# Kernel optimization log

Measured on AMD Instinct MI355X. Metric: run time of the kernel, lower is better.

The kernel has to match this reference:

```python
import jax, jax.numpy as jnp
import numpy as np

HEADS = 16
S = 1024      # affine_dim
B, L = 4, 2048


def _conv1x1(x, W, b):
    # Conv1d with kernel_size=1: pointwise channel mixing. x: (B, C, L)
    return jnp.einsum('oc,bcl->bol', W, x) + b[None, :, None]


def setup_inputs() -> dict:
    key = jax.random.key(0)
    ks = jax.random.split(key, 7)
    scale = 1.0 / np.sqrt(S)  # ~ torch Conv1d default init scale
    return {
        'x':  jax.random.normal(ks[0], (B, S, L), dtype=jnp.float32),
        'Wk': jax.random.normal(ks[1], (S, S), dtype=jnp.float32) * scale,
        'bk': jax.random.normal(ks[2], (S,), dtype=jnp.float32) * scale,
        'Wq': jax.random.normal(ks[3], (S, S), dtype=jnp.float32) * scale,
        'bq': jax.random.normal(ks[4], (S,), dtype=jnp.float32) * scale,
        'Wp': jax.random.normal(ks[5], (S, S), dtype=jnp.float32) * scale,
        'bp': jax.random.normal(ks[6], (S,), dtype=jnp.float32) * scale,
    }


def reference(x, Wk, bk, Wq, bq, Wp, bp):
    b, c, l = x.shape
    h = HEADS
    d = c // h
    keys = _conv1x1(x, Wk, bk).reshape(b, h, d, l)
    queries = _conv1x1(x, Wq, bq).reshape(b, h, d, l)
    # scores[b,h,i,j] = sum_d keys[...,d,i] * queries[...,d,j]  (keys^T @ queries)
    # NOTE: original scales by `seqlen ** 1 / 2` == seqlen / 2 (Python precedence),
    # i.e. multiply by 2/L, NOT 1/sqrt(L). Faithfully preserved.
    scores = jnp.einsum('bhdi,bhdj->bhij', keys, queries) * (2.0 / l)
    attn = jax.nn.softmax(scores, axis=-1)
    xh = x.reshape(b, h, d, l)  # raw x used as values
    out = jnp.einsum('bhdi,bhij->bhdj', xh, attn).reshape(b, c, l)
    return _conv1x1(out, Wp, bp)
```

## Files before the change

kernel.cpp:

```cpp
#include <hip/hip_runtime.h>
#include <hip/hip_bf16.h>
#include <cstdint>
#include <cstddef>

#ifndef __has_builtin
#define __has_builtin(x) 0
#endif

#define DEVI __device__ __forceinline__

typedef __attribute__((ext_vector_type(8))) __bf16 bf16x8;
typedef __attribute__((ext_vector_type(4))) float float4v;
typedef __attribute__((ext_vector_type(16))) float float16v;
typedef __attribute__((ext_vector_type(4))) unsigned short ushort4v;
typedef __attribute__((ext_vector_type(4))) unsigned int uint4v;

constexpr int Bd = 4, Sd = 1024, Ld = 2048, Hd = 16, Dd = 64;

DEVI unsigned short f2bf(float x){
  union { float f; unsigned u; } v; v.f = x;
  unsigned r = v.u + 0x7fffu + ((v.u >> 16) & 1u);
  return (unsigned short)(r >> 16);
}

DEVI unsigned pack2(float lo, float hi){
  union { float f; unsigned u; } a, b; a.f = lo; b.f = hi;
  unsigned ra = a.u + 0x8000u;
  unsigned rb = b.u + 0x8000u;
#if __has_builtin(__builtin_amdgcn_perm)
  return __builtin_amdgcn_perm(rb, ra, 0x07060302u);
#else
  return (ra >> 16) | (rb & 0xffff0000u);
#endif
}

DEVI float fast_exp2(float x){
#if __has_builtin(__builtin_amdgcn_exp2f)
  return __builtin_amdgcn_exp2f(x);
#else
  return exp2f(x);
#endif
}

DEVI void plane32_swap(unsigned &a, unsigned &b){
  asm("v_permlane32_swap_b32 %0, %1" : "+v"(a), "+v"(b));
}

DEVI void gload_lds16(const void* g, void* lds){
  __builtin_amdgcn_global_load_lds(
      (const __attribute__((address_space(1))) void*)g,
      (__attribute__((address_space(3))) void*)lds,
      16, 0, 0);
}

DEVI float4v mfma_bf16(bf16x8 a, bf16x8 b, float4v c){
  return __builtin_amdgcn_mfma_f32_16x16x32_bf16(a, b, c, 0, 0, 0);
}

DEVI float16v mfma32_bf16(bf16x8 a, bf16x8 b, float16v c){
  return __builtin_amdgcn_mfma_f32_32x32x16_bf16(a, b, c, 0, 0, 0);
}


__global__ void wcast_kernel(const float* __restrict__ Wk, const float* __restrict__ Wq,
                             const float* __restrict__ Wp,
                             unsigned short* __restrict__ Wkbf, unsigned short* __restrict__ Wqbf,
                             unsigned short* __restrict__ Wpbf, float ck){
  size_t i = ((size_t)blockIdx.x * 256 + threadIdx.x) * 4;
  float4v a = *(const float4v*)(Wk + i);
  float4v b = *(const float4v*)(Wq + i);
  float4v c = *(const float4v*)(Wp + i);
  ushort4v oa = { f2bf(a[0]*ck), f2bf(a[1]*ck), f2bf(a[2]*ck), f2bf(a[3]*ck) };
  ushort4v ob = { f2bf(b[0]), f2bf(b[1]), f2bf(b[2]), f2bf(b[3]) };
  ushort4v oc = { f2bf(c[0]), f2bf(c[1]), f2bf(c[2]), f2bf(c[3]) };
  *(ushort4v*)(Wkbf + i) = oa;
  *(ushort4v*)(Wqbf + i) = ob;
  *(ushort4v*)(Wpbf + i) = oc;
}

__global__ void transpose_cast(const float* __restrict__ x, unsigned short* __restrict__ Xt){
  __shared__ float tile[32][33];
  const int b = blockIdx.z;
  const int l0 = blockIdx.x * 32;
  const int s0 = blockIdx.y * 32;
  const int tx = threadIdx.x, ty = threadIdx.y;
  #pragma unroll
  for (int r = 0; r < 32; r += 8)
    tile[ty + r][tx] = x[((size_t)b*Sd + s0 + ty + r)*Ld + l0 + tx];
  __syncthreads();
  #pragma unroll
  for (int r = 0; r < 32; r += 8)
    Xt[((size_t)b*Ld + l0 + ty + r)*Sd + s0 + tx] = f2bf(tile[tx][ty + r]);
}

__global__ void vprime_kernel(const float* __restrict__ x, const float* __restrict__ invZ,
                              unsigned short* __restrict__ Vp){
  size_t idx = ((size_t)blockIdx.x * 256 + threadIdx.x) * 4;
  const int l = (int)(idx & (Ld - 1));
  const int c = (int)((idx >> 11) & (Sd - 1));
  const int b = (int)(idx >> 21);
  const int h = c >> 6;
  float4v xv = *(const float4v*)(x + idx);
  float4v zv = *(const float4v*)(invZ + ((size_t)(b*Hd + h) * Ld + l));
  ushort4v o = { f2bf(xv[0]*zv[0]), f2bf(xv[1]*zv[1]), f2bf(xv[2]*zv[2]), f2bf(xv[3]*zv[3]) };
  *(ushort4v*)(Vp + idx) = o;
}

template<int OUT_MODE>
__global__ __launch_bounds__(256, 2)
void conv_gemm(const unsigned short* __restrict__ A,
               const unsigned short* __restrict__ Bt,
               const float* __restrict__ bias, float bscale,
               unsigned short* __restrict__ outT,
               float* __restrict__ outF)
{
  constexpr int BK = 32;
  constexpr int NKSTEP = Sd / BK;
  __shared__ __attribute__((aligned(16))) unsigned short Abuf[2][128*BK];
  __shared__ __attribute__((aligned(16))) unsigned short Bbuf[2][128*BK];

  const int b  = blockIdx.z;
  const int n0 = blockIdx.x * 128;
  const int m0 = blockIdx.y * 128;
  const int tid = threadIdx.x;
  const int w = tid >> 6, lane = tid & 63, lr = lane & 15, lg = lane >> 4;
  const int wm = (w >> 1) * 64, wn = (w & 1) * 64;

  const unsigned short* Abase = A + (size_t)m0 * Sd;
  const unsigned short* Bbase = Bt + ((size_t)b * Ld + n0) * Sd;

  auto stage = [&](int bf, int kt){
    #pragma unroll
    for (int p = 0; p < 2; ++p){
      int slot = p*256 + tid;
      int row = slot >> 2, c = slot & 3;
      int csrc = c ^ ((row >> 1) & 3);
      gload_lds16(Abase + (size_t)row * Sd + kt*BK + csrc*8,
                  (void*)(&Abuf[bf][(size_t)(p*256 + w*64) * 8]));
    }
    #pragma unroll
    for (int p = 0; p < 2; ++p){
      int slot = p*256 + tid;
      int row = slot >> 2, c = slot & 3;
      int csrc = c ^ ((row >> 1) & 3);
      gload_lds16(Bbase + (size_t)row * Sd + kt*BK + csrc*8,
                  (void*)(&Bbuf[bf][(size_t)(p*256 + w*64) * 8]));
    }
  };

  const int gsw = lg ^ ((lr >> 1) & 3);

  float4v acc[4][4];
  #pragma unroll
  for (int i = 0; i < 4; ++i)
    #pragma unroll
    for (int j = 0; j < 4; ++j)
      acc[i][j] = (float4v){0.f, 0.f, 0.f, 0.f};

  stage(0, 0);
  __syncthreads();
  int cur = 0;
  for (int kt = 0; kt < NKSTEP; ++kt){
    if (kt + 1 < NKSTEP) stage(cur ^ 1, kt + 1);
    bf16x8 af[4], bfv[4];
    #pragma unroll
    for (int i = 0; i < 4; ++i){
      int row = wm + i*16 + lr;
      af[i] = *(const bf16x8*)((const char*)&Abuf[cur][0] + (size_t)row*64 + gsw*16);
    }
    #pragma unroll
    for (int j = 0; j < 4; ++j){
      int row = wn + j*16 + lr;
      bfv[j] = *(const bf16x8*)((const char*)&Bbuf[cur][0] + (size_t)row*64 + gsw*16);
    }
    #pragma unroll
    for (int i = 0; i < 4; ++i)
      #pragma unroll
      for (int j = 0; j < 4; ++j)
        acc[i][j] = mfma_bf16(af[i], bfv[j], acc[i][j]);
    __syncthreads();
    cur ^= 1;
  }

  #pragma unroll
  for (int i = 0; i < 4; ++i){
    const int mb = m0 + wm + i*16 + lg*4;
    float4v bv = *(const float4v*)(bias + mb);
    #pragma unroll
    for (int j = 0; j < 4; ++j){
      const int n = n0 + wn + j*16 + lr;
      float4v v = acc[i][j];
      float o0 = v[0] + bscale*bv[0];
      float o1 = v[1] + bscale*bv[1];
      float o2 = v[2] + bscale*bv[2];
      float o3 = v[3] + bscale*bv[3];
      if (OUT_MODE == 0){
        ushort4v o = { f2bf(o0), f2bf(o1), f2bf(o2), f2bf(o3) };
        *(ushort4v*)(outT + ((size_t)b*Ld + n)*Sd + mb) = o;
      } else {
        outF[((size_t)b*Sd + mb + 0)*Ld + n] = o0;
        outF[((size_t)b*Sd + mb + 1)*Ld + n] = o1;
        outF[((size_t)b*Sd + mb + 2)*Ld + n] = o2;
        outF[((size_t)b*Sd + mb + 3)*Ld + n] = o3;
      }
    }
  }
}

__global__ __launch_bounds__(256, 2)
void conv_gemm_kq(const unsigned short* __restrict__ Ak,
                  const unsigned short* __restrict__ Aq,
                  const unsigned short* __restrict__ Bt,
                  const float* __restrict__ bk, const float* __restrict__ bq,
                  float ck,
                  unsigned short* __restrict__ Kt,
                  unsigned short* __restrict__ Qt)
{
  constexpr int BK = 32;
  constexpr int NKSTEP = Sd / BK;
  __shared__ __attribute__((aligned(16))) unsigned short AbufK[2][128*BK];
  __shared__ __attribute__((aligned(16))) unsigned short AbufQ[2][128*BK];
  __shared__ __attribute__((aligned(16))) unsigned short Bbuf[2][128*BK];

  const int b  = blockIdx.z;
  const int n0 = blockIdx.x * 128;
  const int m0 = blockIdx.y * 128;
  const int tid = threadIdx.x;
  const int w = tid >> 6, lane = tid & 63, lr = lane & 15, lg = lane >> 4;
  const int wm = (w >> 1) * 64, wn = (w & 1) * 64;

  const unsigned short* AKbase = Ak + (size_t)m0 * Sd;
  const unsigned short* AQbase = Aq + (size_t)m0 * Sd;
  const unsigned short* Bbase  = Bt + ((size_t)b * Ld + n0) * Sd;

  auto stage = [&](int bf, int kt){
    #pragma unroll
    for (int p = 0; p < 2; ++p){
      int slot = p*256 + tid;
      int row = slot >> 2, c = slot & 3;
      int csrc = c ^ ((row >> 1) & 3);
      const size_t soff = (size_t)row * Sd + kt*BK + csrc*8;
      void* dk = (void*)(&AbufK[bf][(size_t)(p*256 + w*64) * 8]);
      void* dq = (void*)(&AbufQ[bf][(size_t)(p*256 + w*64) * 8]);
      void* db = (void*)(&Bbuf [bf][(size_t)(p*256 + w*64) * 8]);
      gload_lds16(AKbase + soff, dk);
      gload_lds16(AQbase + soff, dq);
      gload_lds16(Bbase  + soff, db);
    }
  };

  const int gsw = lg ^ ((lr >> 1) & 3);

  float4v acck[4][4], accq[4][4];
  #pragma unroll
  for (int i = 0; i < 4; ++i)
    #pragma unroll
    for (int j = 0; j < 4; ++j){
      acck[i][j] = (float4v){0.f, 0.f, 0.f, 0.f};
      accq[i][j] = (float4v){0.f, 0.f, 0.f, 0.f};
    }

  stage(0, 0);
  __syncthreads();
  int cur = 0;
  for (int kt = 0; kt < NKSTEP; ++kt){
    if (kt + 1 < NKSTEP) stage(cur ^ 1, kt + 1);
    bf16x8 afk[4], afq[4], bfv[4];
    #pragma unroll
    for (int i = 0; i < 4; ++i){
      int row = wm + i*16 + lr;
      afk[i] = *(const bf16x8*)((const char*)&AbufK[cur][0] + (size_t)row*64 + gsw*16);
      afq[i] = *(const bf16x8*)((const char*)&AbufQ[cur][0] + (size_t)row*64 + gsw*16);
    }
    #pragma unroll
    for (int j = 0; j < 4; ++j){
      int row = wn + j*16 + lr;
      bfv[j] = *(const bf16x8*)((const char*)&Bbuf[cur][0] + (size_t)row*64 + gsw*16);
    }
    #pragma unroll
    for (int i = 0; i < 4; ++i)
      #pragma unroll
      for (int j = 0; j < 4; ++j){
        acck[i][j] = mfma_bf16(afk[i], bfv[j], acck[i][j]);
        accq[i][j] = mfma_bf16(afq[i], bfv[j], accq[i][j]);
      }
    __syncthreads();
    cur ^= 1;
  }

  #pragma unroll
  for (int i = 0; i < 4; ++i){
    const int mb = m0 + wm + i*16 + lg*4;
    float4v bkv = *(const float4v*)(bk + mb);
    float4v bqv = *(const float4v*)(bq + mb);
    #pragma unroll
    for (int j = 0; j < 4; ++j){
      const int n = n0 + wn + j*16 + lr;
      float4v vk = acck[i][j];
      float4v vq = accq[i][j];
      ushort4v ok = { f2bf(vk[0] + ck*bkv[0]), f2bf(vk[1] + ck*bkv[1]),
                      f2bf(vk[2] + ck*bkv[2]), f2bf(vk[3] + ck*bkv[3]) };
      ushort4v oq = { f2bf(vq[0] + bqv[0]), f2bf(vq[1] + bqv[1]),
                      f2bf(vq[2] + bqv[2]), f2bf(vq[3] + bqv[3]) };
      *(ushort4v*)(Kt + ((size_t)b*Ld + n)*Sd + mb) = ok;
      *(ushort4v*)(Qt + ((size_t)b*Ld + n)*Sd + mb) = oq;
    }
  }
}

__global__ __launch_bounds__(256, 4)
void stats_kernel(const unsigned short* __restrict__ Kt,
                  const unsigned short* __restrict__ Qt,
                  float* __restrict__ invZ)
{
  __shared__ __attribute__((aligned(16))) unsigned short Qbuf[2][64*64];

  const int m = blockIdx.x;
  const int xcd = m & 7, slot = m >> 3;
  const int bh = xcd * 8 + (slot >> 3);
  const int ib = slot & 7;
  const int b = bh >> 4, h = bh & 15;
  const int i0 = ib * 256;

  const int tid = threadIdx.x, w = tid >> 6, lane = tid & 63;
  const int l31 = lane & 31, lh = lane >> 5;
  const int iw0 = i0 + w * 64;

  bf16x8 kb[2][4];
  #pragma unroll
  for (int is = 0; is < 2; ++is)
    #pragma unroll
    for (int ks = 0; ks < 4; ++ks)
      kb[is][ks] = *(const bf16x8*)(Kt + ((size_t)b*Ld + iw0 + is*32 + l31)*Sd + h*64 + ks*16 + lh*8);

  const size_t qbase = (size_t)b*Ld*Sd + (size_t)h*64;
  auto stage = [&](int bf, int jt){
    const int j0 = jt * 64;
    #pragma unroll
    for (int p = 0; p < 2; ++p){
      const int slot2 = p*256 + tid;
      const int row = slot2 >> 3;
      const int gsrc = (slot2 & 7) ^ (row & 7);
      gload_lds16(Qt + qbase + (size_t)(j0 + row)*Sd + gsrc*8,
                  (void*)(&Qbuf[bf][(size_t)slot2 * 8]));
    }
  };

  float z[2] = {0.f, 0.f};
  stage(0, 0);
  __syncthreads();
  int cur = 0;
  for (int jt = 0; jt < 32; ++jt){
    if (jt + 1 < 32) stage(cur ^ 1, jt + 1);
    #pragma unroll
    for (int js = 0; js < 2; ++js){
      bf16x8 qf[4];
      #pragma unroll
      for (int ks = 0; ks < 4; ++ks){
        const int row = js*32 + l31;
        const int g = (2*ks + lh) ^ (l31 & 7);
        qf[ks] = *(const bf16x8*)((const char*)&Qbuf[cur][0] + (size_t)row*128 + g*16);
      }
      #pragma unroll
      for (int is = 0; is < 2; ++is){
        float16v sacc;
        #pragma unroll
        for (int r = 0; r < 16; ++r) sacc[r] = 0.f;
        __builtin_amdgcn_s_setprio(1);
        #pragma unroll
        for (int ks = 0; ks < 4; ++ks)
          sacc = mfma32_bf16(qf[ks], kb[is][ks], sacc);
        __builtin_amdgcn_s_setprio(0);
        #pragma unroll
        for (int r = 0; r < 16; ++r) z[is] += fast_exp2(sacc[r]);
      }
    }
    __syncthreads();
    cur ^= 1;
  }

  #pragma unroll
  for (int is = 0; is < 2; ++is){
    float zv = z[is] + __shfl_xor(z[is], 32, 64);
    if (lh == 0)
      invZ[(size_t)bh * Ld + iw0 + is*32 + l31] = 1.0f / zv;
  }
}

__global__ __launch_bounds__(256, 2)
void attn_pv_kernel(const unsigned short* __restrict__ Kt,
                    const unsigned short* __restrict__ Qt,
                    const unsigned short* __restrict__ Vp,
                    unsigned short* __restrict__ AOt)
{
  __shared__ __attribute__((aligned(16))) unsigned short Kbuf[2][64*64];
  __shared__ __attribute__((aligned(16))) unsigned short Vbuf[2][64*64];

  const int m = blockIdx.x;
  const int xcd = m & 7, slot = m >> 3;
  const int bh = xcd * 8 + (slot >> 3);
  const int jb = slot & 7;
  const int b = bh >> 4, h = bh & 15;
  const int j0 = jb * 256;

  const int tid = threadIdx.x, w = tid >> 6, lane = tid & 63;
  const int l31 = lane & 31, lh = lane >> 5;
  const int jw = j0 + w * 64;

  bf16x8 qb[2][4];
  #pragma unroll
  for (int js = 0; js < 2; ++js)
    #pragma unroll
    for (int ks = 0; ks < 4; ++ks)
      qb[js][ks] = *(const bf16x8*)(Qt + ((size_t)b*Ld + jw + js*32 + l31)*Sd + h*64 + ks*16 + lh*8);

  float16v oacc[2][2];
  #pragma unroll
  for (int ds = 0; ds < 2; ++ds)
    #pragma unroll
    for (int js = 0; js < 2; ++js)
      #pragma unroll
      for (int r = 0; r < 16; ++r) oacc[ds][js][r] = 0.f;

  const size_t kbase = (size_t)b*Ld*Sd + (size_t)h*64;
  const size_t vbase = ((size_t)b*Sd + h*64)*Ld;

  auto stage = [&](int bf, int it){
    const int i0 = it * 64;
    #pragma unroll
    for (int p = 0; p < 2; ++p){
      const int slot2 = p*256 + tid;
      const int row = slot2 >> 3;
      const int gsrc = (slot2 & 7) ^ (row & 7);
      gload_lds16(Kt + kbase + (size_t)(i0 + row)*Sd + gsrc*8,
                  (void*)(&Kbuf[bf][(size_t)slot2 * 8]));
      gload_lds16(Vp + vbase + (size_t)row*Ld + i0 + gsrc*8,
                  (void*)(&Vbuf[bf][(size_t)slot2 * 8]));
    }
  };

  bf16x8 kf[2][4], vf[2][4];
  float16v sacc[2];
  float16v sacc2[2][2];

  auto read_kf = [&](int cb){
    #pragma unroll
    for (int is = 0; is < 2; ++is)
      #pragma unroll
      for (int ks = 0; ks < 4; ++ks){
        const int row = is*32 + l31;
        const int g = (2*ks + lh) ^ (l31 & 7);
        kf[is][ks] = *(const bf16x8*)((const char*)&Kbuf[cb][0] + (size_t)row*128 + g*16);
      }
  };
  auto read_vf = [&](int cb){
    #pragma unroll
    for (int is = 0; is < 2; ++is)
      #pragma unroll
      for (int ks = 0; ks < 4; ++ks){
        const int row = is*32 + l31;
        const int g = (2*ks + lh) ^ (l31 & 7);
        vf[is][ks] = *(const bf16x8*)((const char*)&Vbuf[cb][0] + (size_t)row*128 + g*16);
      }
  };
  auto do_qk = [&](){
    #pragma unroll
    for (int is = 0; is < 2; ++is)
      #pragma unroll
      for (int js = 0; js < 2; ++js)
        #pragma unroll
        for (int r = 0; r < 16; ++r) sacc2[is][js][r] = 0.f;
    __builtin_amdgcn_s_setprio(1);
    #pragma unroll
    for (int js = 0; js < 2; ++js)
      #pragma unroll
      for (int is = 0; is < 2; ++is)
        #pragma unroll
        for (int ks = 0; ks < 4; ++ks)
          sacc2[is][js] = mfma32_bf16(kf[is][ks], qb[js][ks], sacc2[is][js]);
    __builtin_amdgcn_s_setprio(0);
  };
  auto do_exp_pv = [&](){
    #pragma unroll
    for (int js = 0; js < 2; ++js){
      bf16x8 pf[4];
      #pragma unroll
      for (int is = 0; is < 2; ++is){
        #pragma unroll
        for (int hs = 0; hs < 2; ++hs){
          const int r0 = 8*hs;
          unsigned W0 = pack2(fast_exp2(sacc2[is][js][r0+0]), fast_exp2(sacc2[is][js][r0+1]));
          unsigned W1 = pack2(fast_exp2(sacc2[is][js][r0+2]), fast_exp2(sacc2[is][js][r0+3]));
          unsigned W2 = pack2(fast_exp2(sacc2[is][js][r0+4]), fast_exp2(sacc2[is][js][r0+5]));
          unsigned W3 = pack2(fast_exp2(sacc2[is][js][r0+6]), fast_exp2(sacc2[is][js][r0+7]));
          plane32_swap(W0, W2);
          plane32_swap(W1, W3);
          union { uint4v u; bf16x8 v; } cvt;
          cvt.u = (uint4v){ W0, W1, W2, W3 };
          pf[is*2 + hs] = cvt.v;
        }
      }
      __builtin_amdgcn_s_setprio(1);
      #pragma unroll
      for (int kp = 0; kp < 4; ++kp)
        #pragma unroll
        for (int ds = 0; ds < 2; ++ds)
          oacc[ds][js] = mfma32_bf16(vf[ds][kp], pf[kp], oacc[ds][js]);
      __builtin_amdgcn_s_setprio(0);
    }
  };

  stage(0, 0);
  __syncthreads();
  stage(1, 1);
  read_kf(0);
  do_qk();
  read_vf(0);

  for (int t = 0; t < 31; ++t){
    __syncthreads();
    if (t < 30) stage((t) & 1, t + 2);
    read_kf((t + 1) & 1);
    do_exp_pv();
    do_qk();
    read_vf((t + 1) & 1);
  }
  do_exp_pv();

  #pragma unroll
  for (int ds = 0; ds < 2; ++ds)
    #pragma unroll
    for (int js = 0; js < 2; ++js)
      #pragma unroll
      for (int rq = 0; rq < 4; ++rq){
        const int d0 = ds*32 + 8*rq + 4*lh;
        ushort4v o = { f2bf(oacc[ds][js][4*rq+0]), f2bf(oacc[ds][js][4*rq+1]),
                       f2bf(oacc[ds][js][4*rq+2]), f2bf(oacc[ds][js][4*rq+3]) };
        *(ushort4v*)(AOt + ((size_t)b*Ld + jw + js*32 + l31)*Sd + h*64 + d0) = o;
      }
}


extern "C" void kernel_launch(void* const* d_in, const int* in_sizes, int n_in,
                              void* d_out, int out_size, void* d_ws, size_t ws_size,
                              hipStream_t stream)
{
  const float* x  = (const float*)d_in[0];
  const float* Wk = (const float*)d_in[1];
  const float* bk = (const float*)d_in[2];
  const float* Wq = (const float*)d_in[3];
  const float* bq = (const float*)d_in[4];
  const float* Wp = (const float*)d_in[5];
  const float* bp = (const float*)d_in[6];
  float* out = (float*)d_out;

  char* ws = (char*)d_ws;
  const size_t SZ_BLS = (size_t)Bd * Ld * Sd * 2;
  unsigned short* Xt   = (unsigned short*)(ws);
  unsigned short* Kt   = (unsigned short*)(ws + SZ_BLS);
  unsigned short* Qt   = (unsigned short*)(ws + 2*SZ_BLS);
  unsigned short* AOt  = (unsigned short*)(ws + 3*SZ_BLS);
  unsigned short* Wkbf = (unsigned short*)(ws + 4*SZ_BLS);
  unsigned short* Wqbf = (unsigned short*)(ws + 4*SZ_BLS + (size_t)2097152);
  unsigned short* Wpbf = (unsigned short*)(ws + 4*SZ_BLS + (size_t)2*2097152);
  float* invZ          = (float*)(ws + 4*SZ_BLS + (size_t)3*2097152);
  unsigned short* Vp   = Xt;

  const float ck = (2.0f / (float)Ld) * 1.44269504088896f;

  wcast_kernel<<<1024, 256, 0, stream>>>(Wk, Wq, Wp, Wkbf, Wqbf, Wpbf, ck);
  transpose_cast<<<dim3(Ld/32, Sd/32, Bd), dim3(32, 8), 0, stream>>>(x, Xt);

  dim3 cg(Ld/128, Sd/128, Bd);
  conv_gemm_kq<<<cg, 256, 0, stream>>>(Wkbf, Wqbf, Xt, bk, bq, ck, Kt, Qt);

  stats_kernel<<<dim3((Ld/256)*(Bd*Hd)), 256, 0, stream>>>(Kt, Qt, invZ);
  vprime_kernel<<<(Bd*(size_t)Sd*Ld/4)/256, 256, 0, stream>>>(x, invZ, Vp);
  attn_pv_kernel<<<dim3((Ld/256)*(Bd*Hd)), 256, 0, stream>>>(Kt, Qt, Vp, AOt);

  conv_gemm<1><<<cg, 256, 0, stream>>>(Wpbf, AOt, bp, 1.0f, nullptr, out);
}
```

Measured before the change: 218.2 us.

## Split attention over key range into two halves, reduce in projection GEMM

The attention-PV kernel now splits the summation over source positions i into two halves, doubling the grid. Each half writes a separate partial output buffer. The final projection GEMM runs its K loop over both buffers, which sums the partials for free since the projection is linear. This raises parallelism in the attention stage, which had only 512 blocks. The cost is an extra output buffer of workspace traffic, a doubled K loop in the projection GEMM, and bf16 rounding of each partial.

```diff
diff --git a/kernel.cpp b/kernel.cpp
--- a/kernel.cpp
+++ b/kernel.cpp
@@ -106,107 +106,6 @@
   *(ushort4v*)(Vp + idx) = o;
 }
 
-template<int OUT_MODE>
-__global__ __launch_bounds__(256, 2)
-void conv_gemm(const unsigned short* __restrict__ A,
-               const unsigned short* __restrict__ Bt,
-               const float* __restrict__ bias, float bscale,
-               unsigned short* __restrict__ outT,
-               float* __restrict__ outF)
-{
-  constexpr int BK = 32;
-  constexpr int NKSTEP = Sd / BK;
-  __shared__ __attribute__((aligned(16))) unsigned short Abuf[2][128*BK];
-  __shared__ __attribute__((aligned(16))) unsigned short Bbuf[2][128*BK];
-
-  const int b  = blockIdx.z;
-  const int n0 = blockIdx.x * 128;
-  const int m0 = blockIdx.y * 128;
-  const int tid = threadIdx.x;
-  const int w = tid >> 6, lane = tid & 63, lr = lane & 15, lg = lane >> 4;
-  const int wm = (w >> 1) * 64, wn = (w & 1) * 64;
-
-  const unsigned short* Abase = A + (size_t)m0 * Sd;
-  const unsigned short* Bbase = Bt + ((size_t)b * Ld + n0) * Sd;
-
-  auto stage = [&](int bf, int kt){
-    #pragma unroll
-    for (int p = 0; p < 2; ++p){
-      int slot = p*256 + tid;
-      int row = slot >> 2, c = slot & 3;
-      int csrc = c ^ ((row >> 1) & 3);
-      gload_lds16(Abase + (size_t)row * Sd + kt*BK + csrc*8,
-                  (void*)(&Abuf[bf][(size_t)(p*256 + w*64) * 8]));
-    }
-    #pragma unroll
-    for (int p = 0; p < 2; ++p){
-      int slot = p*256 + tid;
-      int row = slot >> 2, c = slot & 3;
-      int csrc = c ^ ((row >> 1) & 3);
-      gload_lds16(Bbase + (size_t)row * Sd + kt*BK + csrc*8,
-                  (void*)(&Bbuf[bf][(size_t)(p*256 + w*64) * 8]));
-    }
-  };
-
-  const int gsw = lg ^ ((lr >> 1) & 3);
-
-  float4v acc[4][4];
-  #pragma unroll
-  for (int i = 0; i < 4; ++i)
-    #pragma unroll
-    for (int j = 0; j < 4; ++j)
-      acc[i][j] = (float4v){0.f, 0.f, 0.f, 0.f};
-
-  stage(0, 0);
-  __syncthreads();
-  int cur = 0;
-  for (int kt = 0; kt < NKSTEP; ++kt){
-    if (kt + 1 < NKSTEP) stage(cur ^ 1, kt + 1);
-    bf16x8 af[4], bfv[4];
-    #pragma unroll
-    for (int i = 0; i < 4; ++i){
-      int row = wm + i*16 + lr;
-      af[i] = *(const bf16x8*)((const char*)&Abuf[cur][0] + (size_t)row*64 + gsw*16);
-    }
-    #pragma unroll
-    for (int j = 0; j < 4; ++j){
-      int row = wn + j*16 + lr;
-      bfv[j] = *(const bf16x8*)((const char*)&Bbuf[cur][0] + (size_t)row*64 + gsw*16);
-    }
-    #pragma unroll
-    for (int i = 0; i < 4; ++i)
-      #pragma unroll
-      for (int j = 0; j < 4; ++j)
-        acc[i][j] = mfma_bf16(af[i], bfv[j], acc[i][j]);
-    __syncthreads();
-    cur ^= 1;
-  }
-
-  #pragma unroll
-  for (int i = 0; i < 4; ++i){
-    const int mb = m0 + wm + i*16 + lg*4;
-    float4v bv = *(const float4v*)(bias + mb);
-    #pragma unroll
-    for (int j = 0; j < 4; ++j){
-      const int n = n0 + wn + j*16 + lr;
-      float4v v = acc[i][j];
-      float o0 = v[0] + bscale*bv[0];
-      float o1 = v[1] + bscale*bv[1];
-      float o2 = v[2] + bscale*bv[2];
-      float o3 = v[3] + bscale*bv[3];
-      if (OUT_MODE == 0){
-        ushort4v o = { f2bf(o0), f2bf(o1), f2bf(o2), f2bf(o3) };
-        *(ushort4v*)(outT + ((size_t)b*Ld + n)*Sd + mb) = o;
-      } else {
-        outF[((size_t)b*Sd + mb + 0)*Ld + n] = o0;
-        outF[((size_t)b*Sd + mb + 1)*Ld + n] = o1;
-        outF[((size_t)b*Sd + mb + 2)*Ld + n] = o2;
-        outF[((size_t)b*Sd + mb + 3)*Ld + n] = o3;
-      }
-    }
-  }
-}
-
 __global__ __launch_bounds__(256, 2)
 void conv_gemm_kq(const unsigned short* __restrict__ Ak,
                   const unsigned short* __restrict__ Aq,
@@ -308,6 +207,93 @@
   }
 }
 
+__global__ __launch_bounds__(256, 2)
+void conv_gemm_p(const unsigned short* __restrict__ A,
+                 const unsigned short* __restrict__ Bt0,
+                 const unsigned short* __restrict__ Bt1,
+                 const float* __restrict__ bias,
+                 float* __restrict__ outF)
+{
+  constexpr int BK = 32;
+  constexpr int NKSTEP = 64;
+  __shared__ __attribute__((aligned(16))) unsigned short Abuf[2][128*BK];
+  __shared__ __attribute__((aligned(16))) unsigned short Bbuf[2][128*BK];
+
+  const int b  = blockIdx.z;
+  const int n0 = blockIdx.x * 128;
+  const int m0 = blockIdx.y * 128;
+  const int tid = threadIdx.x;
+  const int w = tid >> 6, lane = tid & 63, lr = lane & 15, lg = lane >> 4;
+  const int wm = (w >> 1) * 64, wn = (w & 1) * 64;
+
+  const unsigned short* Abase  = A + (size_t)m0 * Sd;
+  const unsigned short* B0base = Bt0 + ((size_t)b * Ld + n0) * Sd;
+  const unsigned short* B1base = Bt1 + ((size_t)b * Ld + n0) * Sd;
+
+  auto stage = [&](int bf, int kt){
+    const int kk = kt & 31;
+    const unsigned short* Bb = (kt < 32) ? B0base : B1base;
+    #pragma unroll
+    for (int p = 0; p < 2; ++p){
+      int slot = p*256 + tid;
+      int row = slot >> 2, c = slot & 3;
+      int csrc = c ^ ((row >> 1) & 3);
+      const size_t soff = (size_t)row * Sd + kk*BK + csrc*8;
+      gload_lds16(Abase + soff, (void*)(&Abuf[bf][(size_t)(p*256 + w*64) * 8]));
+      gload_lds16(Bb    + soff, (void*)(&Bbuf[bf][(size_t)(p*256 + w*64) * 8]));
+    }
+  };
+
+  const int gsw = lg ^ ((lr >> 1) & 3);
+
+  float4v acc[4][4];
+  #pragma unroll
+  for (int i = 0; i < 4; ++i)
+    #pragma unroll
+    for (int j = 0; j < 4; ++j)
+      acc[i][j] = (float4v){0.f, 0.f, 0.f, 0.f};
+
+  stage(0, 0);
+  __syncthreads();
+  int cur = 0;
+  for (int kt = 0; kt < NKSTEP; ++kt){
+    if (kt + 1 < NKSTEP) stage(cur ^ 1, kt + 1);
+    bf16x8 af[4], bfv[4];
+    #pragma unroll
+    for (int i = 0; i < 4; ++i){
+      int row = wm + i*16 + lr;
+      af[i] = *(const bf16x8*)((const char*)&Abuf[cur][0] + (size_t)row*64 + gsw*16);
+    }
+    #pragma unroll
+    for (int j = 0; j < 4; ++j){
+      int row = wn + j*16 + lr;
+      bfv[j] = *(const bf16x8*)((const char*)&Bbuf[cur][0] + (size_t)row*64 + gsw*16);
+    }
+    #pragma unroll
+    for (int i = 0; i < 4; ++i)
+      #pragma unroll
+      for (int j = 0; j < 4; ++j)
+        acc[i][j] = mfma_bf16(af[i], bfv[j], acc[i][j]);
+    __syncthreads();
+    cur ^= 1;
+  }
+
+  #pragma unroll
+  for (int i = 0; i < 4; ++i){
+    const int mb = m0 + wm + i*16 + lg*4;
+    float4v bv = *(const float4v*)(bias + mb);
+    #pragma unroll
+    for (int j = 0; j < 4; ++j){
+      const int n = n0 + wn + j*16 + lr;
+      float4v v = acc[i][j];
+      outF[((size_t)b*Sd + mb + 0)*Ld + n] = v[0] + bv[0];
+      outF[((size_t)b*Sd + mb + 1)*Ld + n] = v[1] + bv[1];
+      outF[((size_t)b*Sd + mb + 2)*Ld + n] = v[2] + bv[2];
+      outF[((size_t)b*Sd + mb + 3)*Ld + n] = v[3] + bv[3];
+    }
+  }
+}
+
 __global__ __launch_bounds__(256, 4)
 void stats_kernel(const unsigned short* __restrict__ Kt,
                   const unsigned short* __restrict__ Qt,
@@ -391,21 +377,26 @@
 void attn_pv_kernel(const unsigned short* __restrict__ Kt,
                     const unsigned short* __restrict__ Qt,
                     const unsigned short* __restrict__ Vp,
-                    unsigned short* __restrict__ AOt)
+                    unsigned short* __restrict__ AOt0,
+                    unsigned short* __restrict__ AOt1)
 {
   __shared__ __attribute__((aligned(16))) unsigned short Kbuf[2][64*64];
   __shared__ __attribute__((aligned(16))) unsigned short Vbuf[2][64*64];
 
   const int m = blockIdx.x;
   const int xcd = m & 7, slot = m >> 3;
-  const int bh = xcd * 8 + (slot >> 3);
+  const int bh = xcd * 8 + (slot >> 4);
+  const int ih = (slot >> 3) & 1;
   const int jb = slot & 7;
   const int b = bh >> 4, h = bh & 15;
   const int j0 = jb * 256;
+  const int it0 = ih * 16;
 
   const int tid = threadIdx.x, w = tid >> 6, lane = tid & 63;
   const int l31 = lane & 31, lh = lane >> 5;
   const int jw = j0 + w * 64;
+
+  unsigned short* AOt = ih ? AOt1 : AOt0;
 
   bf16x8 qb[2][4];
   #pragma unroll
@@ -440,7 +431,6 @@
   };
 
   bf16x8 kf[2][4], vf[2][4];
-  float16v sacc[2];
   float16v sacc2[2][2];
 
   auto read_kf = [&](int cb){
@@ -510,16 +500,16 @@
     }
   };
 
-  stage(0, 0);
+  stage(0, it0 + 0);
   __syncthreads();
-  stage(1, 1);
+  stage(1, it0 + 1);
   read_kf(0);
   do_qk();
   read_vf(0);
 
-  for (int t = 0; t < 31; ++t){
+  for (int t = 0; t < 15; ++t){
     __syncthreads();
-    if (t < 30) stage((t) & 1, t + 2);
+    if (t < 14) stage(t & 1, it0 + t + 2);
     read_kf((t + 1) & 1);
     do_exp_pv();
     do_qk();
@@ -559,11 +549,12 @@
   unsigned short* Xt   = (unsigned short*)(ws);
   unsigned short* Kt   = (unsigned short*)(ws + SZ_BLS);
   unsigned short* Qt   = (unsigned short*)(ws + 2*SZ_BLS);
-  unsigned short* AOt  = (unsigned short*)(ws + 3*SZ_BLS);
-  unsigned short* Wkbf = (unsigned short*)(ws + 4*SZ_BLS);
-  unsigned short* Wqbf = (unsigned short*)(ws + 4*SZ_BLS + (size_t)2097152);
-  unsigned short* Wpbf = (unsigned short*)(ws + 4*SZ_BLS + (size_t)2*2097152);
-  float* invZ          = (float*)(ws + 4*SZ_BLS + (size_t)3*2097152);
+  unsigned short* AOt0 = (unsigned short*)(ws + 3*SZ_BLS);
+  unsigned short* AOt1 = (unsigned short*)(ws + 4*SZ_BLS);
+  unsigned short* Wkbf = (unsigned short*)(ws + 5*SZ_BLS);
+  unsigned short* Wqbf = (unsigned short*)(ws + 5*SZ_BLS + (size_t)2097152);
+  unsigned short* Wpbf = (unsigned short*)(ws + 5*SZ_BLS + (size_t)2*2097152);
+  float* invZ          = (float*)(ws + 5*SZ_BLS + (size_t)3*2097152);
   unsigned short* Vp   = Xt;
 
   const float ck = (2.0f / (float)Ld) * 1.44269504088896f;
@@ -576,7 +567,7 @@
 
   stats_kernel<<<dim3((Ld/256)*(Bd*Hd)), 256, 0, stream>>>(Kt, Qt, invZ);
   vprime_kernel<<<(Bd*(size_t)Sd*Ld/4)/256, 256, 0, stream>>>(x, invZ, Vp);
-  attn_pv_kernel<<<dim3((Ld/256)*(Bd*Hd)), 256, 0, stream>>>(Kt, Qt, Vp, AOt);
-
-  conv_gemm<1><<<cg, 256, 0, stream>>>(Wpbf, AOt, bp, 1.0f, nullptr, out);
-}
+  attn_pv_kernel<<<dim3(2*(Ld/256)*(Bd*Hd)), 256, 0, stream>>>(Kt, Qt, Vp, AOt0, AOt1);
+
+  conv_gemm_p<<<cg, 256, 0, stream>>>(Wpbf, AOt0, AOt1, bp, out);
+}
```

Result: slower. 238.7 us (+9.4%).

## Fuse V-prime scaling into stats kernel and vectorize transpose-cast

Applied to the files above, without the earlier changes.

Removes the separate vprime kernel by having each stats block write its 1/Z values to shared memory and then scale and cast its slice of x into Vp. This eliminates the invZ global buffer round trip and one kernel launch. The transpose kernel also switches to float4 loads and 4-wide bf16 stores with a 1D block. The fused epilogue adds x reads to the stats kernel, which may lengthen its tail.

```diff
diff --git a/kernel.cpp b/kernel.cpp
--- a/kernel.cpp
+++ b/kernel.cpp
@@ -83,27 +83,20 @@
   const int b = blockIdx.z;
   const int l0 = blockIdx.x * 32;
   const int s0 = blockIdx.y * 32;
-  const int tx = threadIdx.x, ty = threadIdx.y;
-  #pragma unroll
-  for (int r = 0; r < 32; r += 8)
-    tile[ty + r][tx] = x[((size_t)b*Sd + s0 + ty + r)*Ld + l0 + tx];
+  const int t = threadIdx.x;
+  {
+    const int r = t >> 3, c4 = (t & 7) * 4;
+    float4v v = *(const float4v*)(x + ((size_t)b*Sd + s0 + r)*Ld + l0 + c4);
+    tile[r][c4+0] = v[0]; tile[r][c4+1] = v[1];
+    tile[r][c4+2] = v[2]; tile[r][c4+3] = v[3];
+  }
   __syncthreads();
-  #pragma unroll
-  for (int r = 0; r < 32; r += 8)
-    Xt[((size_t)b*Ld + l0 + ty + r)*Sd + s0 + tx] = f2bf(tile[tx][ty + r]);
-}
-
-__global__ void vprime_kernel(const float* __restrict__ x, const float* __restrict__ invZ,
-                              unsigned short* __restrict__ Vp){
-  size_t idx = ((size_t)blockIdx.x * 256 + threadIdx.x) * 4;
-  const int l = (int)(idx & (Ld - 1));
-  const int c = (int)((idx >> 11) & (Sd - 1));
-  const int b = (int)(idx >> 21);
-  const int h = c >> 6;
-  float4v xv = *(const float4v*)(x + idx);
-  float4v zv = *(const float4v*)(invZ + ((size_t)(b*Hd + h) * Ld + l));
-  ushort4v o = { f2bf(xv[0]*zv[0]), f2bf(xv[1]*zv[1]), f2bf(xv[2]*zv[2]), f2bf(xv[3]*zv[3]) };
-  *(ushort4v*)(Vp + idx) = o;
+  {
+    const int l = t >> 3, g4 = (t & 7) * 4;
+    ushort4v o = { f2bf(tile[g4+0][l]), f2bf(tile[g4+1][l]),
+                   f2bf(tile[g4+2][l]), f2bf(tile[g4+3][l]) };
+    *(ushort4v*)(Xt + ((size_t)b*Ld + l0 + l)*Sd + s0 + g4) = o;
+  }
 }
 
 template<int OUT_MODE>
@@ -311,9 +304,11 @@
 __global__ __launch_bounds__(256, 4)
 void stats_kernel(const unsigned short* __restrict__ Kt,
                   const unsigned short* __restrict__ Qt,
-                  float* __restrict__ invZ)
+                  const float* __restrict__ x,
+                  unsigned short* __restrict__ Vp)
 {
   __shared__ __attribute__((aligned(16))) unsigned short Qbuf[2][64*64];
+  __shared__ __attribute__((aligned(16))) float zbuf[256];
 
   const int m = blockIdx.x;
   const int xcd = m & 7, slot = m >> 3;
@@ -383,7 +378,21 @@
   for (int is = 0; is < 2; ++is){
     float zv = z[is] + __shfl_xor(z[is], 32, 64);
     if (lh == 0)
-      invZ[(size_t)bh * Ld + iw0 + is*32 + l31] = 1.0f / zv;
+      zbuf[w*64 + is*32 + l31] = 1.0f / zv;
+  }
+  __syncthreads();
+
+  #pragma unroll
+  for (int p = 0; p < 16; ++p){
+    const int e = p*256 + tid;
+    const int d = e >> 6;
+    const int c4 = (e & 63) * 4;
+    const size_t off = ((size_t)b*Sd + h*64 + d)*Ld + i0 + c4;
+    float4v xv = *(const float4v*)(x + off);
+    float4v zv = *(const float4v*)(&zbuf[c4]);
+    ushort4v o = { f2bf(xv[0]*zv[0]), f2bf(xv[1]*zv[1]),
+                   f2bf(xv[2]*zv[2]), f2bf(xv[3]*zv[3]) };
+    *(ushort4v*)(Vp + off) = o;
   }
 }
 
@@ -440,7 +449,6 @@
   };
 
   bf16x8 kf[2][4], vf[2][4];
-  float16v sacc[2];
   float16v sacc2[2][2];
 
   auto read_kf = [&](int cb){
@@ -519,7 +527,7 @@
 
   for (int t = 0; t < 31; ++t){
     __syncthreads();
-    if (t < 30) stage((t) & 1, t + 2);
+    if (t < 30) stage(t & 1, t + 2);
     read_kf((t + 1) & 1);
     do_exp_pv();
     do_qk();
@@ -563,19 +571,17 @@
   unsigned short* Wkbf = (unsigned short*)(ws + 4*SZ_BLS);
   unsigned short* Wqbf = (unsigned short*)(ws + 4*SZ_BLS + (size_t)2097152);
   unsigned short* Wpbf = (unsigned short*)(ws + 4*SZ_BLS + (size_t)2*2097152);
-  float* invZ          = (float*)(ws + 4*SZ_BLS + (size_t)3*2097152);
   unsigned short* Vp   = Xt;
 
   const float ck = (2.0f / (float)Ld) * 1.44269504088896f;
 
   wcast_kernel<<<1024, 256, 0, stream>>>(Wk, Wq, Wp, Wkbf, Wqbf, Wpbf, ck);
-  transpose_cast<<<dim3(Ld/32, Sd/32, Bd), dim3(32, 8), 0, stream>>>(x, Xt);
+  transpose_cast<<<dim3(Ld/32, Sd/32, Bd), 256, 0, stream>>>(x, Xt);
 
   dim3 cg(Ld/128, Sd/128, Bd);
   conv_gemm_kq<<<cg, 256, 0, stream>>>(Wkbf, Wqbf, Xt, bk, bq, ck, Kt, Qt);
 
-  stats_kernel<<<dim3((Ld/256)*(Bd*Hd)), 256, 0, stream>>>(Kt, Qt, invZ);
-  vprime_kernel<<<(Bd*(size_t)Sd*Ld/4)/256, 256, 0, stream>>>(x, invZ, Vp);
+  stats_kernel<<<dim3((Ld/256)*(Bd*Hd)), 256, 0, stream>>>(Kt, Qt, x, Vp);
   attn_pv_kernel<<<dim3((Ld/256)*(Bd*Hd)), 256, 0, stream>>>(Kt, Qt, Vp, AOt);
 
   conv_gemm<1><<<cg, 256, 0, stream>>>(Wpbf, AOt, bp, 1.0f, nullptr, out);
```

Result: no change. 214.9 us (-1.5%).
